# Kernel tuning notes

Hardware: AMD Instinct MI355X
Metric: run time of the kernel (lower is better)

The kernel has to match this reference:

```python
import jax, jax.numpy as jnp
import numpy as np

N = 6000        # nodes
F_IN = 300      # input feature dim
HID = 128       # per-head hidden dim
H = 8           # heads
NEG_INF = -9e15 # mask value used by dense GAT
ALPHA = 0.2     # LeakyReLU slope

# NOTE: dropout (p=0.6) is applied in torch only when training=True; this
# reference implements eval mode, so all dropouts are identity.

def setup_inputs() -> dict:
    key = jax.random.key(0)
    k1, k2, k3, k4, k5, k6 = jax.random.split(key, 6)
    x = jax.random.normal(k1, (N, F_IN), dtype=jnp.float32)
    # sparse-ish 0/1 dense adjacency with self-loops (row-normalizable mask)
    adj = (jax.random.uniform(k2, (N, N)) < 0.05).astype(jnp.float32)
    adj = jnp.maximum(adj, jnp.eye(N, dtype=jnp.float32))
    # per-head params: W ~ xavier_uniform, a ~ xavier_uniform ([2*HID, 1])
    def xavier(k, shape):
        fan_in, fan_out = shape[-2], shape[-1]
        lim = jnp.sqrt(6.0 / (fan_in + fan_out)).astype(jnp.float32)
        return jax.random.uniform(k, shape, jnp.float32, -lim, lim)
    W_heads = xavier(k3, (H, F_IN, HID))          # 8 attention heads
    a_heads = xavier(k4, (H, 2 * HID, 1))
    W_out = xavier(k5, (H * HID, HID))            # final GAT layer
    a_out = xavier(k6, (2 * HID, 1))
    return {"x": x, "adj": adj, "W_heads": W_heads, "a_heads": a_heads,
            "W_out": W_out, "a_out": a_out}


def _masked_softmax(e, adj):
    # attention = softmax over rows, restricted to adj > 0
    return jax.nn.softmax(jnp.where(adj > 0, e, NEG_INF), axis=-1)


def reference(x, adj, W_heads, a_heads, W_out, a_out):
    # ---- multi-head dense GAT layer (concat=True) ----
    Wh = jnp.einsum('nf,hfo->hno', x, W_heads)                    # [H,N,O]
    a1 = a_heads[:, :HID, 0]                                      # [H,O]
    a2 = a_heads[:, HID:, 0]                                      # [H,O]
    f1 = jnp.einsum('hno,ho->hn', Wh, a1)                         # [H,N]
    f2 = jnp.einsum('hno,ho->hn', Wh, a2)                         # [H,N]
    e = jax.nn.leaky_relu(f1[:, :, None] + f2[:, None, :], ALPHA) # [H,N,N]
    attn = _masked_softmax(e, adj[None])                          # [H,N,N]
    h = jax.nn.elu(jnp.einsum('hnm,hmo->hno', attn, Wh))          # [H,N,O]
    hcat = jnp.transpose(h, (1, 0, 2)).reshape(N, H * HID)        # [N,H*O]

    # ---- final GAT layer (concat=False, no elu) ----
    Wh2 = hcat @ W_out                                            # [N,O]
    g1 = (Wh2 @ a_out[:HID]).squeeze(-1)                          # [N]
    g2 = (Wh2 @ a_out[HID:]).squeeze(-1)                          # [N]
    e2 = jax.nn.leaky_relu(g1[:, None] + g2[None, :], ALPHA)      # [N,N]
    attn2 = _masked_softmax(e2, adj)                              # [N,N]
    out = attn2 @ Wh2                                             # [N,O]
    return out
```

## Files before the change

### kernel.cpp

```cpp
#include <hip/hip_runtime.h>
#include <hip/hip_fp16.h>
#include <math.h>

#define N 6000
#define FIN 300
#define HID 128
#define NH 8
#define ALPHA 0.2f
#define NBR_CAP 512
#define KSPLIT 8

typedef unsigned short u16;
typedef unsigned int u32;

static __device__ __forceinline__ u16 f2bf(float f) {
    u32 u = __float_as_uint(f);
    u32 r = (u + 0x7fff + ((u >> 16) & 1)) >> 16;
    return (u16)r;
}
static __device__ __forceinline__ u16 f2h(float f) {
    return __half_as_ushort(__float2half(f));
}

__global__ void build_nbr(const float* __restrict__ adj,
                          u16* __restrict__ nbr,
                          int* __restrict__ ncnt) {
    int n = blockIdx.x;
    int t = threadIdx.x;
    int lane = t & 63, w = t >> 6;
    __shared__ u16 lbuf[4][256];
    __shared__ int wc[4];
    const int seg = N / 4;
    int start = w * seg, end = start + seg;
    const float* row = adj + (size_t)n * N;
    int cnt = 0;
    for (int base = start; base < end; base += 256) {
        int m0 = base + 4 * lane;
        float4 v = make_float4(0.f, 0.f, 0.f, 0.f);
        if (m0 < end) v = *(const float4*)(row + m0);
#pragma unroll
        for (int c = 0; c < 4; c++) {
            float vc = (c == 0) ? v.x : (c == 1) ? v.y : (c == 2) ? v.z : v.w;
            bool p = vc > 0.5f;
            unsigned long long mask = __ballot(p);
            if (p) {
                int pos = cnt + __popcll(mask & ((1ull << lane) - 1ull));
                if (pos < 256) lbuf[w][pos] = (u16)(m0 + c);
            }
            cnt += __popcll(mask);
        }
    }
    if (cnt > 256) cnt = 256;
    if (lane == 0) wc[w] = cnt;
    __syncthreads();
    int offset = 0;
    for (int i = 0; i < w; i++) offset += wc[i];
    for (int i = lane; i < cnt; i += 64) {
        int idx = offset + i;
        if (idx < NBR_CAP) nbr[(size_t)n * NBR_CAP + idx] = lbuf[w][i];
    }
    if (t == 0) {
        int total = wc[0] + wc[1] + wc[2] + wc[3];
        ncnt[n] = total < NBR_CAP ? total : NBR_CAP;
    }
}

__global__ void gemm_wh(const float* __restrict__ x,
                        const float* __restrict__ W,
                        const float* __restrict__ a_heads,
                        u16* __restrict__ Whb,
                        float* __restrict__ f1, float* __restrict__ f2) {
    int h = blockIdx.y;
    int n0 = blockIdx.x * 64;
    __shared__ float xs[64][21];
    __shared__ float bs[20][128];
    int t = threadIdx.x;
    int tx = t & 31, ty = t >> 5;
    float acc[8][4] = {};
    for (int k0 = 0; k0 < FIN; k0 += 20) {
        for (int i = t; i < 64 * 20; i += 256) {
            int r = i / 20, c = i - r * 20;
            int n = n0 + r;
            xs[r][c] = (n < N) ? x[(size_t)n * FIN + k0 + c] : 0.f;
        }
        for (int i = t; i < 20 * 128; i += 256) {
            int r = i >> 7, c = i & 127;
            bs[r][c] = W[((size_t)h * FIN + (k0 + r)) * HID + c];
        }
        __syncthreads();
#pragma unroll
        for (int kk = 0; kk < 20; kk++) {
            float b[4];
#pragma unroll
            for (int j = 0; j < 4; j++) b[j] = bs[kk][tx * 4 + j];
#pragma unroll
            for (int i = 0; i < 8; i++) {
                float a = xs[ty * 8 + i][kk];
#pragma unroll
                for (int j = 0; j < 4; j++) acc[i][j] += a * b[j];
            }
        }
        __syncthreads();
    }
    float a1c[4], a2c[4];
#pragma unroll
    for (int j = 0; j < 4; j++) {
        a1c[j] = a_heads[(size_t)h * 2 * HID + tx * 4 + j];
        a2c[j] = a_heads[(size_t)h * 2 * HID + HID + tx * 4 + j];
    }
    for (int i = 0; i < 8; i++) {
        int n = n0 + ty * 8 + i;
        float s1 = 0.f, s2 = 0.f;
#pragma unroll
        for (int j = 0; j < 4; j++) { s1 += acc[i][j] * a1c[j]; s2 += acc[i][j] * a2c[j]; }
        for (int d = 1; d <= 16; d <<= 1) { s1 += __shfl_xor(s1, d); s2 += __shfl_xor(s2, d); }
        if (n < N) {
            size_t ro = ((size_t)h * N + n) * HID + tx * 4;
            ushort4 b4;
            b4.x = f2bf(acc[i][0]); b4.y = f2bf(acc[i][1]);
            b4.z = f2bf(acc[i][2]); b4.w = f2bf(acc[i][3]);
            *(ushort4*)(Whb + ro) = b4;
            if (tx == 0) { f1[h * N + n] = s1; f2[h * N + n] = s2; }
        }
    }
}

__global__ void gat1(const u16* __restrict__ Whb,
                     const float* __restrict__ f1, const float* __restrict__ f2,
                     const u16* __restrict__ nbr,
                     const int* __restrict__ ncnt,
                     float* __restrict__ hcat) {
    int bid = blockIdx.x;
    int h = bid / N, n = bid - h * N;
    int t = threadIdx.x;
    int s = t >> 4, op = t & 15;
    int cnt = ncnt[n];
    const u16* lst = nbr + (size_t)n * NBR_CAP;
    __shared__ float2 wm[NBR_CAP];
    __shared__ float accl[16][16][9];
    __shared__ float swl[16];

    float f1c = f1[h * N + n];
    for (int i = t; i < cnt; i += 256) {
        int m = lst[i];
        float z = f1c + f2[h * N + m];
        z = (z >= 0.f) ? z : ALPHA * z;
        wm[i] = make_float2(__expf(z), __uint_as_float((u32)m << 8));
    }
    __syncthreads();

    const char* base = (const char*)(Whb + (size_t)h * N * HID) + (op << 4);
    float acc[8] = {};
    float sw = 0.f;
    int j = s;
    for (; j + 16 < cnt; j += 32) {
        float2 p0 = wm[j];
        float2 p1 = wm[j + 16];
        const uint4 va = *(const uint4*)(base + __float_as_uint(p0.y));
        const uint4 vb = *(const uint4*)(base + __float_as_uint(p1.y));
        float w0 = p0.x, w1 = p1.x;
        acc[0] += w0 * __uint_as_float(va.x << 16);
        acc[1] += w0 * __uint_as_float(va.x);
        acc[2] += w0 * __uint_as_float(va.y << 16);
        acc[3] += w0 * __uint_as_float(va.y);
        acc[4] += w0 * __uint_as_float(va.z << 16);
        acc[5] += w0 * __uint_as_float(va.z);
        acc[6] += w0 * __uint_as_float(va.w << 16);
        acc[7] += w0 * __uint_as_float(va.w);
        acc[0] += w1 * __uint_as_float(vb.x << 16);
        acc[1] += w1 * __uint_as_float(vb.x);
        acc[2] += w1 * __uint_as_float(vb.y << 16);
        acc[3] += w1 * __uint_as_float(vb.y);
        acc[4] += w1 * __uint_as_float(vb.z << 16);
        acc[5] += w1 * __uint_as_float(vb.z);
        acc[6] += w1 * __uint_as_float(vb.w << 16);
        acc[7] += w1 * __uint_as_float(vb.w);
        sw += w0 + w1;
    }
    if (j < cnt) {
        float2 p0 = wm[j];
        const uint4 va = *(const uint4*)(base + __float_as_uint(p0.y));
        float w0 = p0.x;
        acc[0] += w0 * __uint_as_float(va.x << 16);
        acc[1] += w0 * __uint_as_float(va.x);
        acc[2] += w0 * __uint_as_float(va.y << 16);
        acc[3] += w0 * __uint_as_float(va.y);
        acc[4] += w0 * __uint_as_float(va.z << 16);
        acc[5] += w0 * __uint_as_float(va.z);
        acc[6] += w0 * __uint_as_float(va.w << 16);
        acc[7] += w0 * __uint_as_float(va.w);
        sw += w0;
    }
#pragma unroll
    for (int c = 0; c < 8; c++) accl[s][op][c] = acc[c];
    if (op == 0) swl[s] = sw;
    __syncthreads();

    if (t < 128) {
        int c = t;
        float r = 0.f;
#pragma unroll
        for (int k = 0; k < 16; k++) r += accl[k][c >> 3][c & 7];
        float swt = 0.f;
#pragma unroll
        for (int k = 0; k < 16; k++) swt += swl[k];
        r /= swt;
        r = (r > 0.f) ? r : expm1f(r);
        hcat[(size_t)n * (NH * HID) + h * HID + c] = r;
    }
}

__global__ void gemm_out(const float* __restrict__ hcat,
                         const float* __restrict__ W_out,
                         float* __restrict__ partial) {
    int n0 = blockIdx.x * 64;
    int ks = blockIdx.y;
    __shared__ float xs[64][17];
    __shared__ float bs[16][128];
    int t = threadIdx.x;
    int tx = t & 31, ty = t >> 5;
    float acc[8][4] = {};
    int kbeg = ks * 128, kend = kbeg + 128;
    for (int k0 = kbeg; k0 < kend; k0 += 16) {
        for (int i = t; i < 64 * 16; i += 256) {
            int r = i >> 4, c = i & 15;
            int n = n0 + r;
            xs[r][c] = (n < N) ? hcat[(size_t)n * 1024 + k0 + c] : 0.f;
        }
        for (int i = t; i < 16 * 128; i += 256) {
            int r = i >> 7, c = i & 127;
            bs[r][c] = W_out[(size_t)(k0 + r) * HID + c];
        }
        __syncthreads();
#pragma unroll
        for (int kk = 0; kk < 16; kk++) {
            float b[4];
#pragma unroll
            for (int j = 0; j < 4; j++) b[j] = bs[kk][tx * 4 + j];
#pragma unroll
            for (int i = 0; i < 8; i++) {
                float a = xs[ty * 8 + i][kk];
#pragma unroll
                for (int j = 0; j < 4; j++) acc[i][j] += a * b[j];
            }
        }
        __syncthreads();
    }
    float* pout = partial + (size_t)ks * N * HID;
    for (int i = 0; i < 8; i++) {
        int n = n0 + ty * 8 + i;
        if (n < N) {
#pragma unroll
            for (int j = 0; j < 4; j++)
                pout[(size_t)n * HID + tx * 4 + j] = acc[i][j];
        }
    }
}

__global__ void reduce_wh2(const float* __restrict__ partial,
                           const float* __restrict__ a_out,
                           u16* __restrict__ Wh2h,
                           float* __restrict__ g1, float* __restrict__ g2) {
    int idx = blockIdx.x * 256 + threadIdx.x;
    float4 v = *(const float4*)(partial + 4 * (size_t)idx);
#pragma unroll
    for (int s = 1; s < KSPLIT; s++) {
        const float4 q = *(const float4*)(partial + (size_t)s * N * HID + 4 * (size_t)idx);
        v.x += q.x; v.y += q.y; v.z += q.z; v.w += q.w;
    }
    ushort4 h4;
    h4.x = f2h(v.x); h4.y = f2h(v.y); h4.z = f2h(v.z); h4.w = f2h(v.w);
    *(ushort4*)(Wh2h + 4 * (size_t)idx) = h4;

    int row = idx >> 5, cg = idx & 31;
    float p1 = v.x * a_out[4 * cg] + v.y * a_out[4 * cg + 1]
             + v.z * a_out[4 * cg + 2] + v.w * a_out[4 * cg + 3];
    float p2 = v.x * a_out[HID + 4 * cg] + v.y * a_out[HID + 4 * cg + 1]
             + v.z * a_out[HID + 4 * cg + 2] + v.w * a_out[HID + 4 * cg + 3];
    for (int d = 1; d <= 16; d <<= 1) { p1 += __shfl_xor(p1, d); p2 += __shfl_xor(p2, d); }
    if ((threadIdx.x & 31) == 0) { g1[row] = p1; g2[row] = p2; }
}

__global__ void gat2(const u16* __restrict__ Wh2h,
                     const float* __restrict__ g1, const float* __restrict__ g2,
                     const u16* __restrict__ nbr,
                     const int* __restrict__ ncnt,
                     float* __restrict__ out) {
    int n = blockIdx.x, t = threadIdx.x;
    int s = t >> 4, op = t & 15;
    int cnt = ncnt[n];
    const u16* lst = nbr + (size_t)n * NBR_CAP;
    __shared__ float2 wm[NBR_CAP];
    __shared__ float accl[16][16][9];
    __shared__ float swl[16];

    float g1c = g1[n];
    for (int i = t; i < cnt; i += 256) {
        int m = lst[i];
        float z = g1c + g2[m];
        z = (z >= 0.f) ? z : ALPHA * z;
        wm[i] = make_float2(__expf(z), __uint_as_float((u32)m << 8));
    }
    __syncthreads();

    const char* base = (const char*)Wh2h + (op << 4);
    float acc[8] = {};
    float sw = 0.f;
    int j = s;
    for (; j + 16 < cnt; j += 32) {
        float2 p0 = wm[j];
        float2 p1 = wm[j + 16];
        const uint4 va = *(const uint4*)(base + __float_as_uint(p0.y));
        const uint4 vb = *(const uint4*)(base + __float_as_uint(p1.y));
        float w0 = p0.x, w1 = p1.x;
        acc[0] += w0 * __half2float(__ushort_as_half((u16)(va.x & 0xffff)));
        acc[1] += w0 * __half2float(__ushort_as_half((u16)(va.x >> 16)));
        acc[2] += w0 * __half2float(__ushort_as_half((u16)(va.y & 0xffff)));
        acc[3] += w0 * __half2float(__ushort_as_half((u16)(va.y >> 16)));
        acc[4] += w0 * __half2float(__ushort_as_half((u16)(va.z & 0xffff)));
        acc[5] += w0 * __half2float(__ushort_as_half((u16)(va.z >> 16)));
        acc[6] += w0 * __half2float(__ushort_as_half((u16)(va.w & 0xffff)));
        acc[7] += w0 * __half2float(__ushort_as_half((u16)(va.w >> 16)));
        acc[0] += w1 * __half2float(__ushort_as_half((u16)(vb.x & 0xffff)));
        acc[1] += w1 * __half2float(__ushort_as_half((u16)(vb.x >> 16)));
        acc[2] += w1 * __half2float(__ushort_as_half((u16)(vb.y & 0xffff)));
        acc[3] += w1 * __half2float(__ushort_as_half((u16)(vb.y >> 16)));
        acc[4] += w1 * __half2float(__ushort_as_half((u16)(vb.z & 0xffff)));
        acc[5] += w1 * __half2float(__ushort_as_half((u16)(vb.z >> 16)));
        acc[6] += w1 * __half2float(__ushort_as_half((u16)(vb.w & 0xffff)));
        acc[7] += w1 * __half2float(__ushort_as_half((u16)(vb.w >> 16)));
        sw += w0 + w1;
    }
    if (j < cnt) {
        float2 p0 = wm[j];
        const uint4 va = *(const uint4*)(base + __float_as_uint(p0.y));
        float w0 = p0.x;
        acc[0] += w0 * __half2float(__ushort_as_half((u16)(va.x & 0xffff)));
        acc[1] += w0 * __half2float(__ushort_as_half((u16)(va.x >> 16)));
        acc[2] += w0 * __half2float(__ushort_as_half((u16)(va.y & 0xffff)));
        acc[3] += w0 * __half2float(__ushort_as_half((u16)(va.y >> 16)));
        acc[4] += w0 * __half2float(__ushort_as_half((u16)(va.z & 0xffff)));
        acc[5] += w0 * __half2float(__ushort_as_half((u16)(va.z >> 16)));
        acc[6] += w0 * __half2float(__ushort_as_half((u16)(va.w & 0xffff)));
        acc[7] += w0 * __half2float(__ushort_as_half((u16)(va.w >> 16)));
        sw += w0;
    }
#pragma unroll
    for (int c = 0; c < 8; c++) accl[s][op][c] = acc[c];
    if (op == 0) swl[s] = sw;
    __syncthreads();

    if (t < 128) {
        int c = t;
        float r = 0.f;
#pragma unroll
        for (int k = 0; k < 16; k++) r += accl[k][c >> 3][c & 7];
        float swt = 0.f;
#pragma unroll
        for (int k = 0; k < 16; k++) swt += swl[k];
        out[(size_t)n * HID + c] = r / swt;
    }
}

extern "C" void kernel_launch(void* const* d_in, const int* in_sizes, int n_in,
                              void* d_out, int out_size, void* d_ws, size_t ws_size,
                              hipStream_t stream) {
    const float* x       = (const float*)d_in[0];
    const float* adj     = (const float*)d_in[1];
    const float* W_heads = (const float*)d_in[2];
    const float* a_heads = (const float*)d_in[3];
    const float* W_out   = (const float*)d_in[4];
    const float* a_out   = (const float*)d_in[5];
    float* out = (float*)d_out;

    char* wsb = (char*)d_ws;
    size_t off = 0;
    auto alloc = [&](size_t bytes) {
        void* p = wsb + off;
        off += (bytes + 255) & ~(size_t)255;
        return p;
    };
    float* partial = (float*)alloc(sizeof(float) * (size_t)KSPLIT * N * HID);
    u16*   Whb  = (u16*)  alloc(sizeof(u16)   * (size_t)NH * N * HID);
    float* hcat = (float*)alloc(sizeof(float) * (size_t)N * NH * HID);
    u16*   Wh2h = (u16*)  alloc(sizeof(u16)   * (size_t)N * HID);
    float* f1   = (float*)alloc(sizeof(float) * (size_t)NH * N);
    float* f2   = (float*)alloc(sizeof(float) * (size_t)NH * N);
    float* g1   = (float*)alloc(sizeof(float) * (size_t)N);
    float* g2   = (float*)alloc(sizeof(float) * (size_t)N);
    u16* nbr    = (u16*)  alloc(sizeof(u16)   * (size_t)N * NBR_CAP);
    int* ncnt   = (int*)  alloc(sizeof(int)   * (size_t)N);

    hipLaunchKernelGGL(build_nbr, dim3(N), dim3(256), 0, stream, adj, nbr, ncnt);
    hipLaunchKernelGGL(gemm_wh, dim3((N + 63) / 64, NH), dim3(256), 0, stream,
                       x, W_heads, a_heads, Whb, f1, f2);
    hipLaunchKernelGGL(gat1, dim3(NH * N), dim3(256), 0, stream, Whb, f1, f2, nbr, ncnt, hcat);
    hipLaunchKernelGGL(gemm_out, dim3((N + 63) / 64, KSPLIT), dim3(256), 0, stream,
                       hcat, W_out, partial);
    hipLaunchKernelGGL(reduce_wh2, dim3(N * HID / 4 / 256), dim3(256), 0, stream,
                       partial, a_out, Wh2h, g1, g2);
    hipLaunchKernelGGL(gat2, dim3(N), dim3(256), 0, stream, Wh2h, g1, g2, nbr, ncnt, out);
}
```

Before: 344.9 us.

## Replace per-node sparse gather aggregation with tiled dense bf16 MFMA attention

The first-layer attention aggregation no longer does per-(head,node) sparse gathers of neighbor rows. It now builds 128-row by 64-column bf16 tiles of unnormalized attention weights in shared memory and multiplies them against a transposed Wh chunk using 16x16x32 bf16 MFMA. gemm_wh now writes Wh transposed (head, channel, node) so B tiles load contiguously. build_nbr also issues four ballots at once instead of four sequential ballot steps. The MFMA path does dense work over all 6000 columns even though the adjacency is about 5% full, runs only 376 blocks, and fills each P tile with a serial per-thread loop. Rounding the attention weights to bf16 also slightly changes the numerics.

```diff
diff --git a/kernel.cpp b/kernel.cpp
--- a/kernel.cpp
+++ b/kernel.cpp
@@ -9,9 +9,14 @@
 #define ALPHA 0.2f
 #define NBR_CAP 512
 #define KSPLIT 8
+#define TM 128
+#define KC 64
+#define NCH ((N + KC - 1) / KC)
 
 typedef unsigned short u16;
 typedef unsigned int u32;
+typedef short bf16x8 __attribute__((ext_vector_type(8)));
+typedef float f32x4 __attribute__((ext_vector_type(4)));
 
 static __device__ __forceinline__ u16 f2bf(float f) {
     u32 u = __float_as_uint(f);
@@ -38,17 +43,19 @@
         int m0 = base + 4 * lane;
         float4 v = make_float4(0.f, 0.f, 0.f, 0.f);
         if (m0 < end) v = *(const float4*)(row + m0);
-#pragma unroll
-        for (int c = 0; c < 4; c++) {
-            float vc = (c == 0) ? v.x : (c == 1) ? v.y : (c == 2) ? v.z : v.w;
-            bool p = vc > 0.5f;
-            unsigned long long mask = __ballot(p);
-            if (p) {
-                int pos = cnt + __popcll(mask & ((1ull << lane) - 1ull));
-                if (pos < 256) lbuf[w][pos] = (u16)(m0 + c);
-            }
-            cnt += __popcll(mask);
-        }
+        bool p0 = v.x > 0.5f, p1 = v.y > 0.5f, p2 = v.z > 0.5f, p3 = v.w > 0.5f;
+        unsigned long long mk0 = __ballot(p0);
+        unsigned long long mk1 = __ballot(p1);
+        unsigned long long mk2 = __ballot(p2);
+        unsigned long long mk3 = __ballot(p3);
+        unsigned long long below = (1ull << lane) - 1ull;
+        int off = cnt + __popcll(mk0 & below) + __popcll(mk1 & below)
+                      + __popcll(mk2 & below) + __popcll(mk3 & below);
+        if (p0) { if (off < 256) lbuf[w][off] = (u16)(m0 + 0); off++; }
+        if (p1) { if (off < 256) lbuf[w][off] = (u16)(m0 + 1); off++; }
+        if (p2) { if (off < 256) lbuf[w][off] = (u16)(m0 + 2); off++; }
+        if (p3) { if (off < 256) lbuf[w][off] = (u16)(m0 + 3); off++; }
+        cnt += __popcll(mk0) + __popcll(mk1) + __popcll(mk2) + __popcll(mk3);
     }
     if (cnt > 256) cnt = 256;
     if (lane == 0) wc[w] = cnt;
@@ -68,7 +75,7 @@
 __global__ void gemm_wh(const float* __restrict__ x,
                         const float* __restrict__ W,
                         const float* __restrict__ a_heads,
-                        u16* __restrict__ Whb,
+                        u16* __restrict__ WhbT,
                         float* __restrict__ f1, float* __restrict__ f2) {
     int h = blockIdx.y;
     int n0 = blockIdx.x * 64;
@@ -114,99 +121,152 @@
 #pragma unroll
         for (int j = 0; j < 4; j++) { s1 += acc[i][j] * a1c[j]; s2 += acc[i][j] * a2c[j]; }
         for (int d = 1; d <= 16; d <<= 1) { s1 += __shfl_xor(s1, d); s2 += __shfl_xor(s2, d); }
-        if (n < N) {
-            size_t ro = ((size_t)h * N + n) * HID + tx * 4;
-            ushort4 b4;
-            b4.x = f2bf(acc[i][0]); b4.y = f2bf(acc[i][1]);
-            b4.z = f2bf(acc[i][2]); b4.w = f2bf(acc[i][3]);
-            *(ushort4*)(Whb + ro) = b4;
-            if (tx == 0) { f1[h * N + n] = s1; f2[h * N + n] = s2; }
-        }
-    }
-}
-
-__global__ void gat1(const u16* __restrict__ Whb,
-                     const float* __restrict__ f1, const float* __restrict__ f2,
-                     const u16* __restrict__ nbr,
-                     const int* __restrict__ ncnt,
-                     float* __restrict__ hcat) {
-    int bid = blockIdx.x;
-    int h = bid / N, n = bid - h * N;
+        if (n < N && tx == 0) { f1[h * N + n] = s1; f2[h * N + n] = s2; }
+    }
+    bool fast = (n0 + 64 <= N);
+#pragma unroll
+    for (int j = 0; j < 4; j++) {
+        int c = tx * 4 + j;
+        u16* dst = WhbT + ((size_t)h * HID + c) * N + n0 + ty * 8;
+        if (fast) {
+            u32 w0 = (u32)f2bf(acc[0][j]) | ((u32)f2bf(acc[1][j]) << 16);
+            u32 w1 = (u32)f2bf(acc[2][j]) | ((u32)f2bf(acc[3][j]) << 16);
+            u32 w2 = (u32)f2bf(acc[4][j]) | ((u32)f2bf(acc[5][j]) << 16);
+            u32 w3 = (u32)f2bf(acc[6][j]) | ((u32)f2bf(acc[7][j]) << 16);
+            *(uint4*)dst = make_uint4(w0, w1, w2, w3);
+        } else {
+            for (int i = 0; i < 8; i++)
+                if (n0 + ty * 8 + i < N) dst[i] = f2bf(acc[i][j]);
+        }
+    }
+}
+
+__global__ __launch_bounds__(256)
+void gat1_mfma(const u16* __restrict__ WhbT,
+               const float* __restrict__ f1, const float* __restrict__ f2,
+               const u16* __restrict__ nbr, const int* __restrict__ ncnt,
+               float* __restrict__ hcat) {
+    int tile = blockIdx.x, h = blockIdx.y;
+    int n0 = tile * TM;
     int t = threadIdx.x;
-    int s = t >> 4, op = t & 15;
-    int cnt = ncnt[n];
-    const u16* lst = nbr + (size_t)n * NBR_CAP;
-    __shared__ float2 wm[NBR_CAP];
-    __shared__ float accl[16][16][9];
-    __shared__ float swl[16];
-
-    float f1c = f1[h * N + n];
-    for (int i = t; i < cnt; i += 256) {
-        int m = lst[i];
-        float z = f1c + f2[h * N + m];
-        z = (z >= 0.f) ? z : ALPHA * z;
-        wm[i] = make_float2(__expf(z), __uint_as_float((u32)m << 8));
-    }
+    int lane = t & 63, wid = t >> 6;
+    int l4 = lane >> 4;
+    int lr = lane & 15;
+
+    __shared__ u16 Pl[TM][KC + 8];
+    __shared__ u16 Bt[HID][KC + 8];
+    __shared__ float swl[TM];
+
+    int cnt = 0;
+    const u16* lst = nullptr;
+    float f1c = 0.f;
+    if (t < TM) {
+        int nrow = n0 + t;
+        if (nrow < N) {
+            cnt = ncnt[nrow];
+            lst = nbr + (size_t)nrow * NBR_CAP;
+            f1c = f1[h * N + nrow];
+        }
+    }
+    int p = 0;
+    float sw = 0.f;
+    const float* f2p = f2 + (size_t)h * N;
+    const u16* wsrc = WhbT + (size_t)h * HID * N;
+
+    f32x4 acc[2][8];
+#pragma unroll
+    for (int rt = 0; rt < 2; rt++)
+#pragma unroll
+        for (int ct = 0; ct < 8; ct++)
+            acc[rt][ct] = (f32x4){0.f, 0.f, 0.f, 0.f};
+
+    for (int ch = 0; ch < NCH; ch++) {
+        int m0 = ch * KC, mend = m0 + KC;
+        {
+            int c = t >> 1, seg = t & 1;
+            int mb = m0 + seg * 32;
+            const u16* src = wsrc + (size_t)c * N + mb;
+            if (mb + 32 <= N) {
+                uint4 v0 = ((const uint4*)src)[0];
+                uint4 v1 = ((const uint4*)src)[1];
+                uint4 v2 = ((const uint4*)src)[2];
+                uint4 v3 = ((const uint4*)src)[3];
+                *(uint4*)&Bt[c][seg * 32 + 0]  = v0;
+                *(uint4*)&Bt[c][seg * 32 + 8]  = v1;
+                *(uint4*)&Bt[c][seg * 32 + 16] = v2;
+                *(uint4*)&Bt[c][seg * 32 + 24] = v3;
+            } else {
+                for (int j = 0; j < 32; j++)
+                    Bt[c][seg * 32 + j] = (mb + j < N) ? src[j] : (u16)0;
+            }
+        }
+        if (t < TM) {
+#pragma unroll
+            for (int j = 0; j < 8; j++)
+                *(uint4*)&Pl[t][8 * j] = make_uint4(0u, 0u, 0u, 0u);
+            while (p < cnt) {
+                int mloc[8];
+                float zv[8];
+                int k = 0;
+#pragma unroll
+                for (int j = 0; j < 8; j++) {
+                    int idx = p + j;
+                    mloc[j] = (idx < cnt) ? (int)lst[idx] : 0x7fffffff;
+                }
+#pragma unroll
+                for (int j = 0; j < 8; j++) {
+                    bool ok = mloc[j] < mend;
+                    zv[j] = ok ? f2p[mloc[j]] : 0.f;
+                    k += ok ? 1 : 0;
+                }
+#pragma unroll
+                for (int j = 0; j < 8; j++) {
+                    if (mloc[j] < mend) {
+                        float z = f1c + zv[j];
+                        z = (z >= 0.f) ? z : ALPHA * z;
+                        u16 bw = f2bf(__expf(z));
+                        Pl[t][mloc[j] - m0] = bw;
+                        sw += __uint_as_float((u32)bw << 16);
+                    }
+                }
+                p += k;
+                if (k < 8) break;
+            }
+        }
+        __syncthreads();
+#pragma unroll
+        for (int ks = 0; ks < 2; ks++) {
+            int kb = ks * 32 + 8 * l4;
+            bf16x8 a0 = *(const bf16x8*)&Pl[32 * wid + lr][kb];
+            bf16x8 a1 = *(const bf16x8*)&Pl[32 * wid + 16 + lr][kb];
+#pragma unroll
+            for (int ct = 0; ct < 8; ct++) {
+                bf16x8 b = *(const bf16x8*)&Bt[16 * ct + lr][kb];
+                acc[0][ct] = __builtin_amdgcn_mfma_f32_16x16x32_bf16(a0, b, acc[0][ct], 0, 0, 0);
+                acc[1][ct] = __builtin_amdgcn_mfma_f32_16x16x32_bf16(a1, b, acc[1][ct], 0, 0, 0);
+            }
+        }
+        __syncthreads();
+    }
+    if (t < TM) swl[t] = sw;
     __syncthreads();
-
-    const char* base = (const char*)(Whb + (size_t)h * N * HID) + (op << 4);
-    float acc[8] = {};
-    float sw = 0.f;
-    int j = s;
-    for (; j + 16 < cnt; j += 32) {
-        float2 p0 = wm[j];
-        float2 p1 = wm[j + 16];
-        const uint4 va = *(const uint4*)(base + __float_as_uint(p0.y));
-        const uint4 vb = *(const uint4*)(base + __float_as_uint(p1.y));
-        float w0 = p0.x, w1 = p1.x;
-        acc[0] += w0 * __uint_as_float(va.x << 16);
-        acc[1] += w0 * __uint_as_float(va.x);
-        acc[2] += w0 * __uint_as_float(va.y << 16);
-        acc[3] += w0 * __uint_as_float(va.y);
-        acc[4] += w0 * __uint_as_float(va.z << 16);
-        acc[5] += w0 * __uint_as_float(va.z);
-        acc[6] += w0 * __uint_as_float(va.w << 16);
-        acc[7] += w0 * __uint_as_float(va.w);
-        acc[0] += w1 * __uint_as_float(vb.x << 16);
-        acc[1] += w1 * __uint_as_float(vb.x);
-        acc[2] += w1 * __uint_as_float(vb.y << 16);
-        acc[3] += w1 * __uint_as_float(vb.y);
-        acc[4] += w1 * __uint_as_float(vb.z << 16);
-        acc[5] += w1 * __uint_as_float(vb.z);
-        acc[6] += w1 * __uint_as_float(vb.w << 16);
-        acc[7] += w1 * __uint_as_float(vb.w);
-        sw += w0 + w1;
-    }
-    if (j < cnt) {
-        float2 p0 = wm[j];
-        const uint4 va = *(const uint4*)(base + __float_as_uint(p0.y));
-        float w0 = p0.x;
-        acc[0] += w0 * __uint_as_float(va.x << 16);
-        acc[1] += w0 * __uint_as_float(va.x);
-        acc[2] += w0 * __uint_as_float(va.y << 16);
-        acc[3] += w0 * __uint_as_float(va.y);
-        acc[4] += w0 * __uint_as_float(va.z << 16);
-        acc[5] += w0 * __uint_as_float(va.z);
-        acc[6] += w0 * __uint_as_float(va.w << 16);
-        acc[7] += w0 * __uint_as_float(va.w);
-        sw += w0;
-    }
-#pragma unroll
-    for (int c = 0; c < 8; c++) accl[s][op][c] = acc[c];
-    if (op == 0) swl[s] = sw;
-    __syncthreads();
-
-    if (t < 128) {
-        int c = t;
-        float r = 0.f;
-#pragma unroll
-        for (int k = 0; k < 16; k++) r += accl[k][c >> 3][c & 7];
-        float swt = 0.f;
-#pragma unroll
-        for (int k = 0; k < 16; k++) swt += swl[k];
-        r /= swt;
-        r = (r > 0.f) ? r : expm1f(r);
-        hcat[(size_t)n * (NH * HID) + h * HID + c] = r;
+#pragma unroll
+    for (int rt = 0; rt < 2; rt++) {
+#pragma unroll
+        for (int reg = 0; reg < 4; reg++) {
+            int rl = 32 * wid + 16 * rt + 4 * l4 + reg;
+            int n = n0 + rl;
+            if (n < N) {
+                float inv = 1.f / swl[rl];
+                float* orow = hcat + (size_t)n * (NH * HID) + h * HID;
+#pragma unroll
+                for (int ct = 0; ct < 8; ct++) {
+                    float v = acc[rt][ct][reg] * inv;
+                    v = (v > 0.f) ? v : expm1f(v);
+                    orow[16 * ct + lr] = v;
+                }
+            }
+        }
     }
 }
 
@@ -381,7 +441,7 @@
         return p;
     };
     float* partial = (float*)alloc(sizeof(float) * (size_t)KSPLIT * N * HID);
-    u16*   Whb  = (u16*)  alloc(sizeof(u16)   * (size_t)NH * N * HID);
+    u16*   WhbT = (u16*)  alloc(sizeof(u16)   * (size_t)NH * HID * N);
     float* hcat = (float*)alloc(sizeof(float) * (size_t)N * NH * HID);
     u16*   Wh2h = (u16*)  alloc(sizeof(u16)   * (size_t)N * HID);
     float* f1   = (float*)alloc(sizeof(float) * (size_t)NH * N);
@@ -393,8 +453,9 @@
 
     hipLaunchKernelGGL(build_nbr, dim3(N), dim3(256), 0, stream, adj, nbr, ncnt);
     hipLaunchKernelGGL(gemm_wh, dim3((N + 63) / 64, NH), dim3(256), 0, stream,
-                       x, W_heads, a_heads, Whb, f1, f2);
-    hipLaunchKernelGGL(gat1, dim3(NH * N), dim3(256), 0, stream, Whb, f1, f2, nbr, ncnt, hcat);
+                       x, W_heads, a_heads, WhbT, f1, f2);
+    hipLaunchKernelGGL(gat1_mfma, dim3((N + TM - 1) / TM, NH), dim3(256), 0, stream,
+                       WhbT, f1, f2, nbr, ncnt, hcat);
     hipLaunchKernelGGL(gemm_out, dim3((N + 63) / 64, KSPLIT), dim3(256), 0, stream,
                        hcat, W_out, partial);
     hipLaunchKernelGGL(reduce_wh2, dim3(N * HID / 4 / 256), dim3(256), 0, stream,
```

Result: slower. 509.1 us (+47.6%).

## Use bf16 MFMA for output GEMM with bf16 hcat and transposed W_out

Applied to the files above, without the earlier changes.

Replaces the scalar fp32 SIMT output projection GEMM with a bf16 MFMA 16x16x32 kernel. It adds a prep kernel that transposes W_out and converts it to bf16, and loads it into XOR-swizzled LDS. gat1 now writes hcat as bf16, which halves that intermediate's memory traffic. KSPLIT drops to 4 so each block covers more K, which also halves the partial-sum buffer that the reduce step reads. The trade-off is reduced precision in the second layer's input and one extra small kernel launch.

```diff
diff --git a/kernel.cpp b/kernel.cpp
--- a/kernel.cpp
+++ b/kernel.cpp
@@ -8,10 +8,12 @@
 #define NH 8
 #define ALPHA 0.2f
 #define NBR_CAP 512
-#define KSPLIT 8
+#define KSPLIT 4
 
 typedef unsigned short u16;
 typedef unsigned int u32;
+typedef short bf16x8 __attribute__((ext_vector_type(8)));
+typedef float f32x4 __attribute__((ext_vector_type(4)));
 
 static __device__ __forceinline__ u16 f2bf(float f) {
     u32 u = __float_as_uint(f);
@@ -125,11 +127,18 @@
     }
 }
 
+__global__ void prep_wout(const float* __restrict__ W_out,
+                          u16* __restrict__ WoT) {
+    int idx = blockIdx.x * 256 + threadIdx.x;
+    int k = idx & 1023, c = idx >> 10;
+    WoT[(size_t)c * 1024 + k] = f2bf(W_out[(size_t)k * HID + c]);
+}
+
 __global__ void gat1(const u16* __restrict__ Whb,
                      const float* __restrict__ f1, const float* __restrict__ f2,
                      const u16* __restrict__ nbr,
                      const int* __restrict__ ncnt,
-                     float* __restrict__ hcat) {
+                     u16* __restrict__ hcatb) {
     int bid = blockIdx.x;
     int h = bid / N, n = bid - h * N;
     int t = threadIdx.x;
@@ -206,53 +215,66 @@
         for (int k = 0; k < 16; k++) swt += swl[k];
         r /= swt;
         r = (r > 0.f) ? r : expm1f(r);
-        hcat[(size_t)n * (NH * HID) + h * HID + c] = r;
-    }
-}
-
-__global__ void gemm_out(const float* __restrict__ hcat,
-                         const float* __restrict__ W_out,
-                         float* __restrict__ partial) {
+        hcatb[(size_t)n * (NH * HID) + h * HID + c] = f2bf(r);
+    }
+}
+
+__global__ __launch_bounds__(256)
+void gemm_out_mfma(const u16* __restrict__ hcatb,
+                   const u16* __restrict__ WoT,
+                   float* __restrict__ partial) {
     int n0 = blockIdx.x * 64;
     int ks = blockIdx.y;
-    __shared__ float xs[64][17];
-    __shared__ float bs[16][128];
     int t = threadIdx.x;
-    int tx = t & 31, ty = t >> 5;
-    float acc[8][4] = {};
-    int kbeg = ks * 128, kend = kbeg + 128;
-    for (int k0 = kbeg; k0 < kend; k0 += 16) {
-        for (int i = t; i < 64 * 16; i += 256) {
-            int r = i >> 4, c = i & 15;
-            int n = n0 + r;
-            xs[r][c] = (n < N) ? hcat[(size_t)n * 1024 + k0 + c] : 0.f;
-        }
-        for (int i = t; i < 16 * 128; i += 256) {
-            int r = i >> 7, c = i & 127;
-            bs[r][c] = W_out[(size_t)(k0 + r) * HID + c];
+    int lane = t & 63, wid = t >> 6;
+    int l4 = lane >> 4, lr = lane & 15;
+
+    __shared__ u16 Bt[128][128];
+
+    f32x4 acc[8];
+#pragma unroll
+    for (int ct = 0; ct < 8; ct++) acc[ct] = (f32x4){0.f, 0.f, 0.f, 0.f};
+
+    int arow = n0 + 16 * wid + lr;
+    const u16* asrc = hcatb + (size_t)arow * (NH * HID);
+    bool avalid = (arow < N);
+
+    for (int half = 0; half < 2; half++) {
+        int kbeg = ks * 256 + half * 128;
+        {
+            int c = t >> 1, sh = t & 1;
+            const u16* src = WoT + (size_t)c * 1024 + kbeg + sh * 64;
+            int cx = (c & 7) << 3;
+            uint4 v[8];
+#pragma unroll
+            for (int j = 0; j < 8; j++) v[j] = ((const uint4*)src)[j];
+#pragma unroll
+            for (int j = 0; j < 8; j++)
+                *(uint4*)&Bt[c][(sh * 64 + 8 * j) ^ cx] = v[j];
         }
         __syncthreads();
 #pragma unroll
-        for (int kk = 0; kk < 16; kk++) {
-            float b[4];
-#pragma unroll
-            for (int j = 0; j < 4; j++) b[j] = bs[kk][tx * 4 + j];
-#pragma unroll
-            for (int i = 0; i < 8; i++) {
-                float a = xs[ty * 8 + i][kk];
-#pragma unroll
-                for (int j = 0; j < 4; j++) acc[i][j] += a * b[j];
+        for (int kst = 0; kst < 4; kst++) {
+            int kb = kst * 32 + 8 * l4;
+            bf16x8 a = {0, 0, 0, 0, 0, 0, 0, 0};
+            if (avalid) a = *(const bf16x8*)(asrc + kbeg + kb);
+#pragma unroll
+            for (int ct = 0; ct < 8; ct++) {
+                int brow = 16 * ct + lr;
+                bf16x8 b = *(const bf16x8*)&Bt[brow][kb ^ ((brow & 7) << 3)];
+                acc[ct] = __builtin_amdgcn_mfma_f32_16x16x32_bf16(a, b, acc[ct], 0, 0, 0);
             }
         }
         __syncthreads();
     }
     float* pout = partial + (size_t)ks * N * HID;
-    for (int i = 0; i < 8; i++) {
-        int n = n0 + ty * 8 + i;
+#pragma unroll
+    for (int reg = 0; reg < 4; reg++) {
+        int n = n0 + 16 * wid + 4 * l4 + reg;
         if (n < N) {
 #pragma unroll
-            for (int j = 0; j < 4; j++)
-                pout[(size_t)n * HID + tx * 4 + j] = acc[i][j];
+            for (int ct = 0; ct < 8; ct++)
+                pout[(size_t)n * HID + 16 * ct + lr] = acc[ct][reg];
         }
     }
 }
@@ -382,7 +404,8 @@
     };
     float* partial = (float*)alloc(sizeof(float) * (size_t)KSPLIT * N * HID);
     u16*   Whb  = (u16*)  alloc(sizeof(u16)   * (size_t)NH * N * HID);
-    float* hcat = (float*)alloc(sizeof(float) * (size_t)N * NH * HID);
+    u16*   hcatb= (u16*)  alloc(sizeof(u16)   * (size_t)N * NH * HID);
+    u16*   WoT  = (u16*)  alloc(sizeof(u16)   * (size_t)HID * 1024);
     u16*   Wh2h = (u16*)  alloc(sizeof(u16)   * (size_t)N * HID);
     float* f1   = (float*)alloc(sizeof(float) * (size_t)NH * N);
     float* f2   = (float*)alloc(sizeof(float) * (size_t)NH * N);
@@ -394,9 +417,10 @@
     hipLaunchKernelGGL(build_nbr, dim3(N), dim3(256), 0, stream, adj, nbr, ncnt);
     hipLaunchKernelGGL(gemm_wh, dim3((N + 63) / 64, NH), dim3(256), 0, stream,
                        x, W_heads, a_heads, Whb, f1, f2);
-    hipLaunchKernelGGL(gat1, dim3(NH * N), dim3(256), 0, stream, Whb, f1, f2, nbr, ncnt, hcat);
-    hipLaunchKernelGGL(gemm_out, dim3((N + 63) / 64, KSPLIT), dim3(256), 0, stream,
-                       hcat, W_out, partial);
+    hipLaunchKernelGGL(prep_wout, dim3(512), dim3(256), 0, stream, W_out, WoT);
+    hipLaunchKernelGGL(gat1, dim3(NH * N), dim3(256), 0, stream, Whb, f1, f2, nbr, ncnt, hcatb);
+    hipLaunchKernelGGL(gemm_out_mfma, dim3((N + 63) / 64, KSPLIT), dim3(256), 0, stream,
+                       hcatb, WoT, partial);
     hipLaunchKernelGGL(reduce_wh2, dim3(N * HID / 4 / 256), dim3(256), 0, stream,
                        partial, a_out, Wh2h, g1, g2);
     hipLaunchKernelGGL(gat2, dim3(N), dim3(256), 0, stream, Wh2h, g1, g2, nbr, ncnt, out);
```

After: 321.2 us. 6.9% less time.
